# Performance work log

Measured on AMD Instinct MI355X. Metric: run time of the kernel, lower is better.

Reference implementation:

```python
import jax, jax.numpy as jnp
import numpy as np

NUM_CLS = 80
NUM_CONVS = 4
GROUPS = 32
STRIDES = [8, 16, 32, 64, 128]
SIZES = [32.0, 64.0, 128.0, 256.0, 512.0]
CLS_BIAS_INIT = -float(np.log((1 - 0.01) / 0.01))


def _conv(x, w, b):
    # NCHW 3x3 stride-1 same-pad conv
    y = jax.lax.conv_general_dilated(x, w, (1, 1), 'SAME',
                                     dimension_numbers=('NCHW', 'OIHW', 'NCHW'))
    return y + b[None, :, None, None]


def _group_norm(x, gamma, beta, eps=1e-5):
    B, C, H, W = x.shape
    xr = x.reshape(B, GROUPS, C // GROUPS, H, W)
    m = xr.mean(axis=(2, 3, 4), keepdims=True)
    v = xr.var(axis=(2, 3, 4), keepdims=True)
    xn = ((xr - m) / jnp.sqrt(v + eps)).reshape(B, C, H, W)
    return xn * gamma[None, :, None, None] + beta[None, :, None, None]


def _tower(x, ws, bs, gs, betas):
    # CGR block: Conv -> GroupNorm -> ReLU, repeated NUM_CONVS times
    for i in range(NUM_CONVS):
        x = jax.nn.relu(_group_norm(_conv(x, ws[i], bs[i]), gs[i], betas[i]))
    return x


def _build_anchors(h, w, stride, size):
    half = size / 2.0  # single scale=1, ratio=1 -> one square anchor per cell
    yv, xv = jnp.meshgrid(jnp.arange(h, dtype=jnp.float32),
                          jnp.arange(w, dtype=jnp.float32), indexing='ij')
    grid = jnp.stack([xv, yv, xv, yv], axis=-1)  # [h,w,4]
    delta = jnp.array([-half, -half, half, half], dtype=jnp.float32)
    return ((grid + 0.5) * stride + delta).reshape(-1, 4)  # [h*w,4]


def setup_inputs() -> dict:
    key = jax.random.key(0)
    ks = jax.random.split(key, 16)
    C = 256
    feats = {}
    hw = [80, 40, 20, 10, 5]
    for i, name in enumerate(['p3', 'p4', 'p5', 'p6', 'p7']):
        feats[name] = jax.random.normal(ks[i], (8, C, hw[i], hw[i]), dtype=jnp.float32)
    std = 0.01
    inp = dict(feats)
    # cls tower
    inp['cls_tw'] = jax.random.normal(ks[5], (NUM_CONVS, C, C, 3, 3), jnp.float32) * std
    inp['cls_tb'] = jnp.zeros((NUM_CONVS, C), jnp.float32)
    inp['cls_tg'] = jnp.ones((NUM_CONVS, C), jnp.float32)
    inp['cls_tbeta'] = jnp.zeros((NUM_CONVS, C), jnp.float32)
    # reg tower
    inp['reg_tw'] = jax.random.normal(ks[6], (NUM_CONVS, C, C, 3, 3), jnp.float32) * std
    inp['reg_tb'] = jnp.zeros((NUM_CONVS, C), jnp.float32)
    inp['reg_tg'] = jnp.ones((NUM_CONVS, C), jnp.float32)
    inp['reg_tbeta'] = jnp.zeros((NUM_CONVS, C), jnp.float32)
    # heads (num_anchors = 1)
    inp['cls_hw'] = jax.random.normal(ks[7], (NUM_CLS, C, 3, 3), jnp.float32) * std
    inp['cls_hb'] = jnp.full((NUM_CLS,), CLS_BIAS_INIT, jnp.float32)
    inp['reg_hw'] = jax.random.normal(ks[8], (4, C, 3, 3), jnp.float32) * std
    inp['reg_hb'] = jnp.zeros((4,), jnp.float32)
    inp['iou_hw'] = jax.random.normal(ks[9], (1, C, 3, 3), jnp.float32) * std
    inp['iou_hb'] = jnp.zeros((1,), jnp.float32)
    inp['scales'] = jnp.ones((5,), jnp.float32)
    return inp


def reference(p3, p4, p5, p6, p7,
              cls_tw, cls_tb, cls_tg, cls_tbeta,
              reg_tw, reg_tb, reg_tg, reg_tbeta,
              cls_hw, cls_hb, reg_hw, reg_hb, iou_hw, iou_hb, scales):
    feats = [p3, p4, p5, p6, p7]
    outs = []
    for j, x in enumerate(feats):
        B, _, H, W = x.shape
        ct = _tower(x, cls_tw, cls_tb, cls_tg, cls_tbeta)
        rt = _tower(x, reg_tw, reg_tb, reg_tg, reg_tbeta)
        # heads: permute to NHWC then flatten spatial (num_anchors=1)
        cls = _conv(ct, cls_hw, cls_hb).transpose(0, 2, 3, 1).reshape(B, -1, NUM_CLS)
        reg = _conv(rt, reg_hw, reg_hb).transpose(0, 2, 3, 1).reshape(B, -1, 4) * scales[j]
        iou = _conv(rt, iou_hw, iou_hb).transpose(0, 2, 3, 1).reshape(B, -1, 1)  # on_reg=True
        # decode boxes against anchors
        anchor = _build_anchors(H, W, STRIDES[j], SIZES[j])  # [HW,4]
        awh = anchor[:, 2:] - anchor[:, :2]
        actr = anchor[:, :2] + 0.5 * awh
        xy = reg[..., :2] * awh + actr
        wh = jnp.exp(reg[..., 2:]) * awh
        box = jnp.concatenate([xy - 0.5 * wh, xy + 0.5 * wh], axis=-1)
        outs.append(jnp.concatenate([box, iou, cls], axis=-1))
    return jnp.concatenate(outs, axis=1)  # [B, 8525, 85]
```

## Files before the change

### kernel.cpp

```cpp
#include <hip/hip_runtime.h>
#include <stdint.h>

typedef unsigned short u16;
typedef unsigned int u32;
typedef short short8 __attribute__((ext_vector_type(8)));
typedef float f32x4 __attribute__((ext_vector_type(4)));

struct LevelTab {
  int Hf[5], Wf[5], Hp[5], Wp[5], HW[5], M[5], mtcum[5], aoff[5];
  long xoffp[5], moff[5], ppcum[5], mcum[5];
  float asize[5], astride[5];
};

__device__ __forceinline__ u16 f2bf(float f) {
  u32 u = __float_as_uint(f);
  u = (u + 0x7fffu + ((u >> 16) & 1u)) >> 16;
  return (u16)u;
}
__device__ __forceinline__ float bflo(u32 v) { return __uint_as_float(v << 16); }
__device__ __forceinline__ float bfhi(u32 v) { return __uint_as_float(v & 0xffff0000u); }

__device__ __forceinline__ void gload16(const void* g, void* l) {
  __builtin_amdgcn_global_load_lds((__attribute__((address_space(1))) void*)(g),
                                   (__attribute__((address_space(3))) void*)(l),
                                   16, 0, 0);
}

__global__ __launch_bounds__(256) void prep_tower_w(const float* __restrict__ cls_tw,
                                                    const float* __restrict__ reg_tw,
                                                    u16* __restrict__ W2t) {
  long t = (long)blockIdx.x * 256 + threadIdx.x;
  const long total = 2L * 4 * 256 * 2304;
  if (t >= total) return;
  int ci = (int)(t & 255);
  long u = t >> 8;
  int j = (int)(u % 9); u /= 9;
  int co = (int)(u & 255); u >>= 8;
  int layer = (int)(u & 3);
  int tw = (int)(u >> 2);
  const float* src = tw ? reg_tw : cls_tw;
  float v = src[(((long)layer * 256 + co) * 256 + ci) * 9 + j];
  W2t[t] = f2bf(v);
}

__global__ __launch_bounds__(256) void prep_cls_w(const float* __restrict__ cls_hw,
                                                  u16* __restrict__ W2c) {
  long t = (long)blockIdx.x * 256 + threadIdx.x;
  if (t >= 128L * 2304) return;
  int ci = (int)(t & 255);
  long u = t >> 8;
  int j = (int)(u % 9);
  int co = (int)(u / 9);
  float v = (co < 80) ? cls_hw[(((long)co * 256 + ci) * 9 + j)] : 0.f;
  W2c[t] = f2bf(v);
}

__global__ __launch_bounds__(256) void prep_reg_w(const float* __restrict__ reg_hw,
                                                  const float* __restrict__ iou_hw,
                                                  u16* __restrict__ W2r) {
  long t = (long)blockIdx.x * 256 + threadIdx.x;
  if (t >= 5L * 2304) return;
  int ci = (int)(t & 255);
  long u = t >> 8;
  int j = (int)(u % 9);
  int o = (int)(u / 9);
  float v = (o < 4) ? reg_hw[(((long)o * 256 + ci) * 9 + j)] : iou_hw[(long)ci * 9 + j];
  W2r[t] = f2bf(v);
}

__global__ __launch_bounds__(256) void convert_in(const float* __restrict__ i0, const float* __restrict__ i1,
                                                  const float* __restrict__ i2, const float* __restrict__ i3,
                                                  const float* __restrict__ i4, u16* __restrict__ X0,
                                                  LevelTab lt) {
  long t = (long)blockIdx.x * 256 + threadIdx.x;
  if (t >= lt.ppcum[4] * 32) return;
  const int c8 = (int)(t & 31);
  long pp = t >> 5;
  int lvl = 0;
#pragma unroll
  for (int i = 0; i < 4; ++i) lvl += (pp >= lt.ppcum[i]);
  const long lp = pp - (lvl ? lt.ppcum[lvl - 1] : 0);
  const int Hp = lt.Hp[lvl], Wp = lt.Wp[lvl], Wf = lt.Wf[lvl], HW = lt.HW[lvl];
  const int HpWp = Hp * Wp;
  const int n = (int)(lp / HpWp);
  const int rem = (int)(lp - (long)n * HpWp);
  const int yp = rem / Wp, xp = rem - yp * Wp;
  u16* op = X0 + (lt.xoffp[lvl] + lp) * 256 + c8 * 8;
  if (yp == 0 || yp == Hp - 1 || xp == 0 || xp == Wp - 1) {
    *(uint4*)op = make_uint4(0u, 0u, 0u, 0u);
    return;
  }
  const float* src = lvl == 0 ? i0 : lvl == 1 ? i1 : lvl == 2 ? i2 : lvl == 3 ? i3 : i4;
  const int y = yp - 1, x = xp - 1;
  const long sb = ((long)n * 256 + c8 * 8) * HW + (long)y * Wf + x;
  u32 o4[4];
#pragma unroll
  for (int i = 0; i < 4; ++i) {
    float f0 = src[sb + (long)(2 * i) * HW];
    float f1 = src[sb + (long)(2 * i + 1) * HW];
    o4[i] = (u32)f2bf(f0) | ((u32)f2bf(f1) << 16);
  }
  *(uint4*)op = make_uint4(o4[0], o4[1], o4[2], o4[3]);
}

template <int MODE>
__global__ __launch_bounds__(256, 2) void conv_mfma(const u16* __restrict__ Xpad,
                                                    const u16* __restrict__ W2,
                                                    const float* __restrict__ bias,
                                                    u16* __restrict__ Otmp,
                                                    float* __restrict__ Oout, LevelTab lt) {
  __shared__ __align__(16) u16 sA[3][128 * 32];
  __shared__ __align__(16) u16 sB[3][128 * 32];

  const int nwg = gridDim.x;
  const int qq = nwg >> 3, rr = nwg & 7;
  const int xcd = blockIdx.x & 7, ib = blockIdx.x >> 3;
  const int sid = (xcd < rr ? xcd * (qq + 1) : rr * (qq + 1) + (xcd - rr) * qq) + ib;
  const int tileId = (MODE == 0) ? (sid >> 1) : sid;
  const int nt = (MODE == 0) ? (sid & 1) : 0;

  int lvl = 0;
#pragma unroll
  for (int i = 0; i < 4; ++i) lvl += (tileId >= lt.mtcum[i]);
  const int mt = tileId - (lvl ? lt.mtcum[lvl - 1] : 0);
  const int Hp = lt.Hp[lvl], Wp = lt.Wp[lvl], Wf = lt.Wf[lvl];
  const int HW = lt.HW[lvl], M = lt.M[lvl];
  const long xbase = lt.xoffp[lvl] * 256;

  const int tid = threadIdx.x;
  const int w = tid >> 6, lane = tid & 63;
  const int rsub = lane >> 2;
  const int r0 = w * 16 + rsub;
  const int q2 = ((lane & 3) - ((lane >> 3) & 3)) & 3;

  long gA[2], gB[2];
#pragma unroll
  for (int i = 0; i < 2; ++i) {
    int ml = mt * 128 + r0 + i * 64;
    if (ml > M - 1) ml = M - 1;
    const int n = ml / HW;
    const int pr = ml - n * HW;
    const int y = pr / Wf;
    const int x = pr - y * Wf;
    gA[i] = xbase + ((long)((n * Hp + y) * Wp + x)) * 256 + q2 * 8;
    gB[i] = (long)(nt * 128 + r0 + i * 64) * 2304 + q2 * 8;
  }

  const int wm = w >> 1, wn = w & 1;
  const int lm = lane & 15;
  const int slot8 = ((((lane >> 4) + ((lane >> 1) & 3)) & 3) << 3);

  f32x4 acc[4][4];
#pragma unroll
  for (int a = 0; a < 4; ++a)
#pragma unroll
    for (int c = 0; c < 4; ++c) acc[a][c] = {0.f, 0.f, 0.f, 0.f};

  auto STAGE = [&](int kk, int buf) {
    const int j = kk >> 3;
    const int c0 = (kk & 7) << 5;
    const int jy = j / 3, jx = j - jy * 3;
    const long aK = ((long)(jy * Wp + jx)) * 256 + c0;
    const long bK = (long)kk << 5;
    gload16(Xpad + gA[0] + aK, sA[buf] + w * 512);
    gload16(Xpad + gA[1] + aK, sA[buf] + 2048 + w * 512);
    gload16(W2 + gB[0] + bK, sB[buf] + w * 512);
    gload16(W2 + gB[1] + bK, sB[buf] + 2048 + w * 512);
  };

  short8 af[4], bfv[4];
  auto FRAG = [&](int cur) {
    const u16* pa = sA[cur];
    const u16* pb = sB[cur];
#pragma unroll
    for (int mi = 0; mi < 4; ++mi)
      af[mi] = *(const short8*)(pa + ((wm * 64 + mi * 16 + lm) << 5) + slot8);
#pragma unroll
    for (int ni = 0; ni < 4; ++ni)
      bfv[ni] = *(const short8*)(pb + ((wn * 64 + ni * 16 + lm) << 5) + slot8);
  };
  auto DOMFMA = [&]() {
    __builtin_amdgcn_s_setprio(1);
#pragma unroll
    for (int mi = 0; mi < 4; ++mi)
#pragma unroll
      for (int ni = 0; ni < 4; ++ni)
        acc[mi][ni] =
            __builtin_amdgcn_mfma_f32_16x16x32_bf16(af[mi], bfv[ni], acc[mi][ni], 0, 0, 0);
    __builtin_amdgcn_s_setprio(0);
  };

  STAGE(0, 0);
  STAGE(1, 1);
  int cur = 0;
  for (int kk = 0; kk < 70; ++kk) {
    asm volatile("s_waitcnt vmcnt(4)" ::: "memory");
    __builtin_amdgcn_s_barrier();
    FRAG(cur);
    STAGE(kk + 2, cur == 0 ? 2 : cur - 1);
    DOMFMA();
    cur = cur == 2 ? 0 : cur + 1;
  }
  asm volatile("s_waitcnt vmcnt(4)" ::: "memory");
  __builtin_amdgcn_s_barrier();
  FRAG(cur);
  DOMFMA();
  cur = cur == 2 ? 0 : cur + 1;
  asm volatile("s_waitcnt vmcnt(0)" ::: "memory");
  __builtin_amdgcn_s_barrier();
  FRAG(cur);
  DOMFMA();

  const int mwb = mt * 128 + wm * 64;
  const int colb = nt * 128 + wn * 64;
  const int rq4 = (lane >> 4) << 2;
#pragma unroll
  for (int ni = 0; ni < 4; ++ni) {
    const int col = colb + ni * 16 + lm;
    if (MODE == 1 && col >= 80) continue;
    const float bv = bias[col];
#pragma unroll
    for (int mi = 0; mi < 4; ++mi) {
      const int rb = mwb + mi * 16 + rq4;
#pragma unroll
      for (int rg = 0; rg < 4; ++rg) {
        const int ml = rb + rg;
        if (ml < M) {
          const float v = acc[mi][ni][rg] + bv;
          if (MODE == 0) {
            Otmp[(lt.moff[lvl] + ml) * 256 + col] = f2bf(v);
          } else {
            const int nb = ml / HW;
            const int pr = ml - nb * HW;
            Oout[((long)nb * 8525 + lt.aoff[lvl] + pr) * 85 + 5 + col] = v;
          }
        }
      }
    }
  }
}

__global__ __launch_bounds__(256) void gn_stats(const u16* __restrict__ tmp,
                                                float* __restrict__ stats, LevelTab lt) {
  const int bid = blockIdx.x;
  const int lvl = bid >> 8, bg = bid & 255, b = bg >> 5, g = bg & 31;
  const int HW = lt.HW[lvl];
  const long base = (lt.moff[lvl] + (long)b * HW) * 256 + g * 8;
  float s = 0.f, ss = 0.f;
  for (int p = threadIdx.x; p < HW; p += 256) {
    const uint4 r = *(const uint4*)(tmp + base + (long)p * 256);
    const u32 u[4] = {r.x, r.y, r.z, r.w};
#pragma unroll
    for (int i = 0; i < 4; ++i) {
      float f0 = bflo(u[i]), f1 = bfhi(u[i]);
      s += f0 + f1;
      ss += f0 * f0 + f1 * f1;
    }
  }
#pragma unroll
  for (int o = 32; o; o >>= 1) {
    s += __shfl_down(s, o);
    ss += __shfl_down(ss, o);
  }
  __shared__ float rs[4], rss[4];
  const int w = threadIdx.x >> 6, lane = threadIdx.x & 63;
  if (lane == 0) { rs[w] = s; rss[w] = ss; }
  __syncthreads();
  if (threadIdx.x == 0) {
    s = rs[0] + rs[1] + rs[2] + rs[3];
    ss = rss[0] + rss[1] + rss[2] + rss[3];
    const float inv = 1.f / (float)(HW * 8);
    const float mean = s * inv;
    const float var = ss * inv - mean * mean;
    stats[bid * 2 + 0] = mean;
    stats[bid * 2 + 1] = rsqrtf(var + 1e-5f);
  }
}

__global__ __launch_bounds__(256) void gn_apply(const u16* __restrict__ tmp,
                                                const float* __restrict__ stats,
                                                const float* __restrict__ gamma,
                                                const float* __restrict__ beta,
                                                u16* __restrict__ pout, LevelTab lt) {
  long t = (long)blockIdx.x * 256 + threadIdx.x;
  if (t >= lt.ppcum[4] * 32) return;
  const int c8 = (int)(t & 31);
  long pp = t >> 5;
  int lvl = 0;
#pragma unroll
  for (int i = 0; i < 4; ++i) lvl += (pp >= lt.ppcum[i]);
  const long lp = pp - (lvl ? lt.ppcum[lvl - 1] : 0);
  const int Hp = lt.Hp[lvl], Wp = lt.Wp[lvl], Wf = lt.Wf[lvl], HW = lt.HW[lvl];
  const int HpWp = Hp * Wp;
  const int n = (int)(lp / HpWp);
  const int rem = (int)(lp - (long)n * HpWp);
  const int yp = rem / Wp, xp = rem - yp * Wp;
  u16* op = pout + (lt.xoffp[lvl] + lp) * 256 + c8 * 8;
  if (yp == 0 || yp == Hp - 1 || xp == 0 || xp == Wp - 1) {
    *(uint4*)op = make_uint4(0u, 0u, 0u, 0u);
    return;
  }
  const long m = lt.moff[lvl] + (long)n * HW + (long)(yp - 1) * Wf + (xp - 1);
  const uint4 r = *(const uint4*)(tmp + m * 256 + c8 * 8);
  const int sidx = (lvl * 256 + n * 32 + c8) * 2;
  const float mean = stats[sidx], rstd = stats[sidx + 1];
  const u32 u[4] = {r.x, r.y, r.z, r.w};
  u32 o4[4];
#pragma unroll
  for (int i = 0; i < 4; ++i) {
    const int c = c8 * 8 + i * 2;
    float f0 = (bflo(u[i]) - mean) * rstd * gamma[c] + beta[c];
    float f1 = (bfhi(u[i]) - mean) * rstd * gamma[c + 1] + beta[c + 1];
    f0 = fmaxf(f0, 0.f);
    f1 = fmaxf(f1, 0.f);
    o4[i] = (u32)f2bf(f0) | ((u32)f2bf(f1) << 16);
  }
  *(uint4*)op = make_uint4(o4[0], o4[1], o4[2], o4[3]);
}

__global__ __launch_bounds__(256) void regiou_decode(const u16* __restrict__ Xp,
                                                     const u16* __restrict__ W2r,
                                                     const float* __restrict__ reg_hb,
                                                     const float* __restrict__ iou_hb,
                                                     const float* __restrict__ scales,
                                                     float* __restrict__ out, LevelTab lt) {
  const long gt = (long)blockIdx.x * 256 + threadIdx.x;
  const int gw = (int)(gt >> 6);
  const int lane = threadIdx.x & 63;
  if (gw >= (int)lt.mcum[4]) return;
  int lvl = 0;
#pragma unroll
  for (int i = 0; i < 4; ++i) lvl += (gw >= (int)lt.mcum[i]);
  const int m = gw - (int)(lvl ? lt.mcum[lvl - 1] : 0);
  const int HW = lt.HW[lvl], Wf = lt.Wf[lvl], Hp = lt.Hp[lvl], Wp = lt.Wp[lvl];
  const int b = m / HW, pr = m - b * HW;
  const int y = pr / Wf, x = pr - y * Wf;
  const long base = (lt.xoffp[lvl] + (long)(b * Hp + y) * Wp + x) * 256 + lane * 4;
  float acc[5] = {0.f, 0.f, 0.f, 0.f, 0.f};
#pragma unroll
  for (int j = 0; j < 9; ++j) {
    const int jy = j / 3, jx = j - jy * 3;
    const uint2 ar = *(const uint2*)(Xp + base + ((long)(jy * Wp + jx)) * 256);
    const float x0 = bflo(ar.x), x1 = bfhi(ar.x), x2 = bflo(ar.y), x3 = bfhi(ar.y);
#pragma unroll
    for (int o = 0; o < 5; ++o) {
      const uint2 wr = *(const uint2*)(W2r + o * 2304 + j * 256 + lane * 4);
      acc[o] += x0 * bflo(wr.x) + x1 * bfhi(wr.x) + x2 * bflo(wr.y) + x3 * bfhi(wr.y);
    }
  }
#pragma unroll
  for (int o = 0; o < 5; ++o)
#pragma unroll
    for (int d = 32; d; d >>= 1) acc[o] += __shfl_down(acc[o], d);
  if (lane == 0) {
    const float sc = scales[lvl];
    const float r0 = (acc[0] + reg_hb[0]) * sc;
    const float r1 = (acc[1] + reg_hb[1]) * sc;
    const float r2 = (acc[2] + reg_hb[2]) * sc;
    const float r3 = (acc[3] + reg_hb[3]) * sc;
    const float iou = acc[4] + iou_hb[0];
    const float st = lt.astride[lvl], sz = lt.asize[lvl];
    const float cx = (x + 0.5f) * st, cy = (y + 0.5f) * st;
    const float xx = r0 * sz + cx, yy = r1 * sz + cy;
    const float ww = expf(r2) * sz, hh = expf(r3) * sz;
    float* o = out + ((long)b * 8525 + lt.aoff[lvl] + pr) * 85;
    o[0] = xx - 0.5f * ww;
    o[1] = yy - 0.5f * hh;
    o[2] = xx + 0.5f * ww;
    o[3] = yy + 0.5f * hh;
    o[4] = iou;
  }
}

extern "C" void kernel_launch(void* const* d_in, const int* in_sizes, int n_in, void* d_out,
                              int out_size, void* d_ws, size_t ws_size, hipStream_t stream) {
  const float* feats[5];
  for (int i = 0; i < 5; ++i) feats[i] = (const float*)d_in[i];
  const float* cls_tw = (const float*)d_in[5];
  const float* cls_tb = (const float*)d_in[6];
  const float* cls_tg = (const float*)d_in[7];
  const float* cls_tbeta = (const float*)d_in[8];
  const float* reg_tw = (const float*)d_in[9];
  const float* reg_tb = (const float*)d_in[10];
  const float* reg_tg = (const float*)d_in[11];
  const float* reg_tbeta = (const float*)d_in[12];
  const float* cls_hw = (const float*)d_in[13];
  const float* cls_hb = (const float*)d_in[14];
  const float* reg_hw = (const float*)d_in[15];
  const float* reg_hb = (const float*)d_in[16];
  const float* iou_hw = (const float*)d_in[17];
  const float* iou_hb = (const float*)d_in[18];
  const float* scales = (const float*)d_in[19];
  float* out = (float*)d_out;

  LevelTab lt;
  const int Hs[5] = {80, 40, 20, 10, 5};
  const float sizes[5] = {32.f, 64.f, 128.f, 256.f, 512.f};
  const float strides[5] = {8.f, 16.f, 32.f, 64.f, 128.f};
  long ppc = 0, mc = 0;
  int mtc = 0, ao = 0;
  for (int i = 0; i < 5; ++i) {
    const int H = Hs[i];
    lt.Hf[i] = H; lt.Wf[i] = H; lt.Hp[i] = H + 2; lt.Wp[i] = H + 2;
    lt.HW[i] = H * H; lt.M[i] = 8 * H * H;
    lt.xoffp[i] = ppc; lt.moff[i] = mc; lt.aoff[i] = ao;
    ppc += 8L * (H + 2) * (H + 2);
    mc += lt.M[i];
    mtc += (lt.M[i] + 127) / 128;
    lt.ppcum[i] = ppc; lt.mcum[i] = mc; lt.mtcum[i] = mtc;
    ao += H * H;
    lt.asize[i] = sizes[i]; lt.astride[i] = strides[i];
  }

  char* ws = (char*)d_ws;
  size_t off = 0;
  auto take = [&](size_t bytes) {
    off = (off + 255) & ~(size_t)255;
    char* p = ws + off;
    off += bytes;
    return p;
  };
  u16* X0 = (u16*)take((size_t)ppc * 256 * 2);
  u16* padA = (u16*)take((size_t)ppc * 256 * 2);
  u16* padB = (u16*)take((size_t)ppc * 256 * 2);
  u16* tmp = (u16*)take((size_t)mc * 256 * 2);
  u16* W2t = (u16*)take((size_t)2 * 4 * 256 * 2304 * 2);
  u16* W2c = (u16*)take((size_t)128 * 2304 * 2);
  u16* W2r = (u16*)take((size_t)5 * 2304 * 2);
  float* stats = (float*)take((size_t)5 * 256 * 2 * 4);

  prep_tower_w<<<(int)((2L * 4 * 256 * 2304 + 255) / 256), 256, 0, stream>>>(cls_tw, reg_tw, W2t);
  prep_cls_w<<<(int)((128L * 2304 + 255) / 256), 256, 0, stream>>>(cls_hw, W2c);
  prep_reg_w<<<(int)((5L * 2304 + 255) / 256), 256, 0, stream>>>(reg_hw, iou_hw, W2r);

  const int ppBlocks = (int)((ppc * 32 + 255) / 256);
  convert_in<<<ppBlocks, 256, 0, stream>>>(feats[0], feats[1], feats[2], feats[3], feats[4], X0, lt);

  u16* pads[2] = {padA, padB};
  for (int tw = 0; tw < 2; ++tw) {
    const float* tb = tw ? reg_tb : cls_tb;
    const float* tg = tw ? reg_tg : cls_tg;
    const float* tbe = tw ? reg_tbeta : cls_tbeta;
    const u16* cur = X0;
    for (int layer = 0; layer < 4; ++layer) {
      const u16* w2 = W2t + (size_t)(tw * 4 + layer) * 256 * 2304;
      conv_mfma<0><<<mtc * 2, 256, 0, stream>>>(cur, w2, tb + layer * 256, tmp, nullptr, lt);
      gn_stats<<<5 * 256, 256, 0, stream>>>(tmp, stats, lt);
      u16* nxt = pads[layer & 1];
      gn_apply<<<ppBlocks, 256, 0, stream>>>(tmp, stats, tg + layer * 256, tbe + layer * 256, nxt, lt);
      cur = nxt;
    }
    if (tw == 0) {
      conv_mfma<1><<<mtc, 256, 0, stream>>>(cur, W2c, cls_hb, nullptr, out, lt);
    } else {
      regiou_decode<<<(int)((mc * 64 + 255) / 256), 256, 0, stream>>>(cur, W2r, reg_hb, iou_hb,
                                                                      scales, out, lt);
    }
  }
}
```

Before: 1.562 ms.

## Enlarge conv GEMM tiles to 256 rows with 512-thread blocks

Conv tile grows from 128x128 to 256x256 for the tower layers, computed by 8 waves in a 2x4 layout, and to 256x128 for the class head. The output-channel split across blocks is removed. Each input patch is now loaded once instead of twice, which cuts global/L2 traffic and gives more MFMA work per barrier. The cost is about 96KB LDS and 128 accumulator VGPRs per thread, which lowers occupancy. The grid is also much smaller, risking underfilled CUs and worse latency hiding.

```diff
diff --git a/kernel.cpp b/kernel.cpp
--- a/kernel.cpp
+++ b/kernel.cpp
@@ -104,20 +104,21 @@
 }
 
 template <int MODE>
-__global__ __launch_bounds__(256, 2) void conv_mfma(const u16* __restrict__ Xpad,
+__global__ __launch_bounds__(512, 2) void conv_mfma(const u16* __restrict__ Xpad,
                                                     const u16* __restrict__ W2,
                                                     const float* __restrict__ bias,
                                                     u16* __restrict__ Otmp,
                                                     float* __restrict__ Oout, LevelTab lt) {
-  __shared__ __align__(16) u16 sA[3][128 * 32];
-  __shared__ __align__(16) u16 sB[3][128 * 32];
+  constexpr int NI = (MODE == 0) ? 4 : 2;
+  constexpr int NB = (MODE == 0) ? 2 : 1;
+  constexpr int BN = 64 * NI;
+  __shared__ __align__(16) u16 sA[3][256 * 32];
+  __shared__ __align__(16) u16 sB[3][BN * 32];
 
   const int nwg = gridDim.x;
   const int qq = nwg >> 3, rr = nwg & 7;
   const int xcd = blockIdx.x & 7, ib = blockIdx.x >> 3;
-  const int sid = (xcd < rr ? xcd * (qq + 1) : rr * (qq + 1) + (xcd - rr) * qq) + ib;
-  const int tileId = (MODE == 0) ? (sid >> 1) : sid;
-  const int nt = (MODE == 0) ? (sid & 1) : 0;
+  const int tileId = (xcd < rr ? xcd * (qq + 1) : rr * (qq + 1) + (xcd - rr) * qq) + ib;
 
   int lvl = 0;
 #pragma unroll
@@ -133,28 +134,29 @@
   const int r0 = w * 16 + rsub;
   const int q2 = ((lane & 3) - ((lane >> 3) & 3)) & 3;
 
-  long gA[2], gB[2];
+  long gA[2], gB[NB];
 #pragma unroll
   for (int i = 0; i < 2; ++i) {
-    int ml = mt * 128 + r0 + i * 64;
+    int ml = mt * 256 + r0 + i * 128;
     if (ml > M - 1) ml = M - 1;
     const int n = ml / HW;
     const int pr = ml - n * HW;
     const int y = pr / Wf;
     const int x = pr - y * Wf;
     gA[i] = xbase + ((long)((n * Hp + y) * Wp + x)) * 256 + q2 * 8;
-    gB[i] = (long)(nt * 128 + r0 + i * 64) * 2304 + q2 * 8;
-  }
-
-  const int wm = w >> 1, wn = w & 1;
+  }
+#pragma unroll
+  for (int i = 0; i < NB; ++i) gB[i] = (long)(r0 + i * 128) * 2304 + q2 * 8;
+
+  const int wm = w >> 2, wn = w & 3;
   const int lm = lane & 15;
   const int slot8 = ((((lane >> 4) + ((lane >> 1) & 3)) & 3) << 3);
 
-  f32x4 acc[4][4];
-#pragma unroll
-  for (int a = 0; a < 4; ++a)
-#pragma unroll
-    for (int c = 0; c < 4; ++c) acc[a][c] = {0.f, 0.f, 0.f, 0.f};
+  f32x4 acc[8][NI];
+#pragma unroll
+  for (int a = 0; a < 8; ++a)
+#pragma unroll
+    for (int c = 0; c < NI; ++c) acc[a][c] = {0.f, 0.f, 0.f, 0.f};
 
   auto STAGE = [&](int kk, int buf) {
     const int j = kk >> 3;
@@ -163,28 +165,28 @@
     const long aK = ((long)(jy * Wp + jx)) * 256 + c0;
     const long bK = (long)kk << 5;
     gload16(Xpad + gA[0] + aK, sA[buf] + w * 512);
-    gload16(Xpad + gA[1] + aK, sA[buf] + 2048 + w * 512);
+    gload16(Xpad + gA[1] + aK, sA[buf] + 4096 + w * 512);
     gload16(W2 + gB[0] + bK, sB[buf] + w * 512);
-    gload16(W2 + gB[1] + bK, sB[buf] + 2048 + w * 512);
+    if constexpr (NB == 2) gload16(W2 + gB[1] + bK, sB[buf] + 4096 + w * 512);
   };
 
-  short8 af[4], bfv[4];
+  short8 af[8], bfv[NI];
   auto FRAG = [&](int cur) {
     const u16* pa = sA[cur];
     const u16* pb = sB[cur];
 #pragma unroll
-    for (int mi = 0; mi < 4; ++mi)
-      af[mi] = *(const short8*)(pa + ((wm * 64 + mi * 16 + lm) << 5) + slot8);
-#pragma unroll
-    for (int ni = 0; ni < 4; ++ni)
-      bfv[ni] = *(const short8*)(pb + ((wn * 64 + ni * 16 + lm) << 5) + slot8);
+    for (int mi = 0; mi < 8; ++mi)
+      af[mi] = *(const short8*)(pa + ((wm * 128 + mi * 16 + lm) << 5) + slot8);
+#pragma unroll
+    for (int ni = 0; ni < NI; ++ni)
+      bfv[ni] = *(const short8*)(pb + ((wn * (NI * 16) + ni * 16 + lm) << 5) + slot8);
   };
   auto DOMFMA = [&]() {
     __builtin_amdgcn_s_setprio(1);
 #pragma unroll
-    for (int mi = 0; mi < 4; ++mi)
-#pragma unroll
-      for (int ni = 0; ni < 4; ++ni)
+    for (int mi = 0; mi < 8; ++mi)
+#pragma unroll
+      for (int ni = 0; ni < NI; ++ni)
         acc[mi][ni] =
             __builtin_amdgcn_mfma_f32_16x16x32_bf16(af[mi], bfv[ni], acc[mi][ni], 0, 0, 0);
     __builtin_amdgcn_s_setprio(0);
@@ -194,14 +196,20 @@
   STAGE(1, 1);
   int cur = 0;
   for (int kk = 0; kk < 70; ++kk) {
-    asm volatile("s_waitcnt vmcnt(4)" ::: "memory");
+    if constexpr (MODE == 0)
+      asm volatile("s_waitcnt vmcnt(4)" ::: "memory");
+    else
+      asm volatile("s_waitcnt vmcnt(3)" ::: "memory");
     __builtin_amdgcn_s_barrier();
     FRAG(cur);
     STAGE(kk + 2, cur == 0 ? 2 : cur - 1);
     DOMFMA();
     cur = cur == 2 ? 0 : cur + 1;
   }
-  asm volatile("s_waitcnt vmcnt(4)" ::: "memory");
+  if constexpr (MODE == 0)
+    asm volatile("s_waitcnt vmcnt(4)" ::: "memory");
+  else
+    asm volatile("s_waitcnt vmcnt(3)" ::: "memory");
   __builtin_amdgcn_s_barrier();
   FRAG(cur);
   DOMFMA();
@@ -211,16 +219,16 @@
   FRAG(cur);
   DOMFMA();
 
-  const int mwb = mt * 128 + wm * 64;
-  const int colb = nt * 128 + wn * 64;
+  const int mwb = mt * 256 + wm * 128;
+  const int colb = wn * (NI * 16);
   const int rq4 = (lane >> 4) << 2;
 #pragma unroll
-  for (int ni = 0; ni < 4; ++ni) {
+  for (int ni = 0; ni < NI; ++ni) {
     const int col = colb + ni * 16 + lm;
     if (MODE == 1 && col >= 80) continue;
     const float bv = bias[col];
 #pragma unroll
-    for (int mi = 0; mi < 4; ++mi) {
+    for (int mi = 0; mi < 8; ++mi) {
       const int rb = mwb + mi * 16 + rq4;
 #pragma unroll
       for (int rg = 0; rg < 4; ++rg) {
@@ -406,7 +414,7 @@
     lt.xoffp[i] = ppc; lt.moff[i] = mc; lt.aoff[i] = ao;
     ppc += 8L * (H + 2) * (H + 2);
     mc += lt.M[i];
-    mtc += (lt.M[i] + 127) / 128;
+    mtc += (lt.M[i] + 255) / 256;
     lt.ppcum[i] = ppc; lt.mcum[i] = mc; lt.mtcum[i] = mtc;
     ao += H * H;
     lt.asize[i] = sizes[i]; lt.astride[i] = strides[i];
@@ -444,14 +452,14 @@
     const u16* cur = X0;
     for (int layer = 0; layer < 4; ++layer) {
       const u16* w2 = W2t + (size_t)(tw * 4 + layer) * 256 * 2304;
-      conv_mfma<0><<<mtc * 2, 256, 0, stream>>>(cur, w2, tb + layer * 256, tmp, nullptr, lt);
+      conv_mfma<0><<<mtc, 512, 0, stream>>>(cur, w2, tb + layer * 256, tmp, nullptr, lt);
       gn_stats<<<5 * 256, 256, 0, stream>>>(tmp, stats, lt);
       u16* nxt = pads[layer & 1];
       gn_apply<<<ppBlocks, 256, 0, stream>>>(tmp, stats, tg + layer * 256, tbe + layer * 256, nxt, lt);
       cur = nxt;
     }
     if (tw == 0) {
-      conv_mfma<1><<<mtc, 256, 0, stream>>>(cur, W2c, cls_hb, nullptr, out, lt);
+      conv_mfma<1><<<mtc, 512, 0, stream>>>(cur, W2c, cls_hb, nullptr, out, lt);
     } else {
       regiou_decode<<<(int)((mc * 64 + 255) / 256), 256, 0, stream>>>(cur, W2r, reg_hb, iou_hb,
                                                                       scales, out, lt);
```

Measured after the change: 1.831 ms. 17.2% more time.
